# Performance work log

Hardware: AMD Instinct MI355X
Metric: run time of the kernel (lower is better)

## Reference

```python
import jax, jax.numpy as jnp
import numpy as np

B, SX, SL, D, H = 4, 4096, 256, 1024, 16
DH = D // H
LN_EPS = 1e-5
RMS_EPS = 1e-8


def layernorm(x, g, b):
    mu = jnp.mean(x, axis=-1, keepdims=True)
    var = jnp.mean(jnp.square(x - mu), axis=-1, keepdims=True)
    return (x - mu) * jax.lax.rsqrt(var + LN_EPS) * g + b


def rmsnorm(x, gamma):
    # torch: norm = ||x||_2 * dim^-0.5 ; x / clamp(norm, eps) * gamma
    norm = jnp.sqrt(jnp.sum(jnp.square(x), axis=-1, keepdims=True)) * (DH ** -0.5)
    return x / jnp.maximum(norm, RMS_EPS) * gamma


def setup_inputs() -> dict:
    key = jax.random.key(0)
    ks = jax.random.split(key, 6)
    s = 0.02
    return {
        "x": jax.random.normal(ks[0], (B, SX, D), jnp.float32),
        "latents": jax.random.normal(ks[1], (B, SL, D), jnp.float32),
        "mask_x": jnp.ones((B, SX), jnp.float32),
        "mask_latent": jnp.ones((B, SL), jnp.float32),
        "ln_x_g": jnp.ones((D,), jnp.float32),
        "ln_x_b": jnp.zeros((D,), jnp.float32),
        "ln_l_g": jnp.ones((D,), jnp.float32),
        "ln_l_b": jnp.zeros((D,), jnp.float32),
        "Wq": jax.random.normal(ks[2], (D, D), jnp.float32) * s,
        "Wkv": jax.random.normal(ks[3], (D, 2 * D), jnp.float32) * s,
        "qk_gamma": jnp.ones((DH,), jnp.float32),
        "Wo": jax.random.normal(ks[4], (D, D), jnp.float32) * s,
    }


def reference(x, latents, mask_x, mask_latent, ln_x_g, ln_x_b, ln_l_g, ln_l_b, Wq, Wkv, qk_gamma, Wo):
    xn = layernorm(x, ln_x_g, ln_x_b)                       # [B,SX,D]
    ln = layernorm(latents, ln_l_g, ln_l_b)                 # [B,SL,D]

    q = (ln @ Wq).reshape(B, SL, H, DH).transpose(0, 2, 1, 3)      # [B,H,SL,DH]
    kv_in = jnp.concatenate([xn, ln], axis=1)                      # [B,SX+SL,D]
    kv = kv_in @ Wkv
    Skv = SX + SL
    k = kv[..., :D].reshape(B, Skv, H, DH).transpose(0, 2, 1, 3)   # [B,H,Skv,DH]
    v = kv[..., D:].reshape(B, Skv, H, DH).transpose(0, 2, 1, 3)

    # NOTE: original code applies query_norm to BOTH q and k (faithful to source)
    q = rmsnorm(q, qk_gamma)
    k = rmsnorm(k, qk_gamma)

    scores = jnp.einsum("bhqd,bhkd->bhqk", q, k) / np.sqrt(DH)     # [B,H,SL,Skv]

    kv_mask = jnp.concatenate([mask_x, mask_latent], axis=1)       # [B,Skv]
    mask = kv_mask[:, None, :] * mask_latent[:, :, None]           # [B,SL,Skv]
    add_mask = (1.0 - mask)[:, None, :, :] * jnp.finfo(scores.dtype).min
    attn = jax.nn.softmax(scores + add_mask, axis=-1)

    y = jnp.einsum("bhqk,bhkd->bhqd", attn, v)                     # [B,H,SL,DH]
    y = y.transpose(0, 2, 1, 3).reshape(B, SL, D)
    return y @ Wo
```

## Files before the change

### kernel.cpp

```cpp
#include <hip/hip_runtime.h>

#define NB   4
#define SXX  4096
#define SLL  256
#define DD   1024
#define HH   16
#define DHH  64
#define SKV  4352
#define MKV  17408
#define NSPLIT 8

typedef __attribute__((ext_vector_type(8))) short bfrag;
typedef __attribute__((ext_vector_type(4))) float facc;

__device__ __forceinline__ unsigned short f2bf(float f){
  unsigned u = __builtin_bit_cast(unsigned, f);
  u = (u + 0x7fffu + ((u >> 16) & 1u)) >> 16;
  return (unsigned short)u;
}
__device__ __forceinline__ float bf2f(unsigned short h){
  unsigned u = ((unsigned)h) << 16;
  return __builtin_bit_cast(float, u);
}

#define GLOAD_LDS16(g, lds) __builtin_amdgcn_global_load_lds( \
    (const __attribute__((address_space(1))) unsigned int*)(const void*)(g), \
    (__attribute__((address_space(3))) unsigned int*)(void*)(lds), 16, 0, 0)

__global__ void wtrans3(const float* __restrict__ Wq, const float* __restrict__ Wkv,
                        const float* __restrict__ Wo, unsigned short* __restrict__ wqt,
                        unsigned short* __restrict__ wkvt, unsigned short* __restrict__ wot){
  __shared__ float t[32][33];
  int z = blockIdx.z;
  const float* in; unsigned short* out; int N;
  if (z == 0){ in = Wq;  out = wqt;  N = DD;   }
  else if (z == 1){ in = Wkv; out = wkvt; N = 2*DD; }
  else { in = Wo;  out = wot;  N = DD;   }
  int n0 = blockIdx.x * 32, k0 = blockIdx.y * 32;
  if (n0 >= N) return;
  int tx = threadIdx.x, ty = threadIdx.y;
  #pragma unroll
  for (int i = 0; i < 4; i++)
    t[ty + 8*i][tx] = in[(size_t)(k0 + ty + 8*i) * N + n0 + tx];
  __syncthreads();
  #pragma unroll
  for (int i = 0; i < 4; i++)
    out[(size_t)(n0 + ty + 8*i) * DD + k0 + tx] = f2bf(t[tx][ty + 8*i]);
}

__global__ __launch_bounds__(256) void lnorm2(const float* __restrict__ x,
    const float* __restrict__ lat,
    const float* __restrict__ gx, const float* __restrict__ bx,
    const float* __restrict__ gl, const float* __restrict__ bl,
    unsigned short* __restrict__ kvin, unsigned short* __restrict__ lnlat){
  int t = threadIdx.x, w = t >> 6, l = t & 63;
  int gr = blockIdx.x * 4 + w;
  const float* src; const float* g; const float* bt;
  unsigned short* d2 = nullptr;
  int b, s, off;
  if (gr < NB*SXX){
    b = gr >> 12; s = gr & 4095; off = 0;
    src = x + (size_t)gr * DD; g = gx; bt = bx;
  } else {
    int r = gr - NB*SXX;
    b = r >> 8; s = r & 255; off = SXX;
    src = lat + (size_t)r * DD; g = gl; bt = bl;
    d2 = lnlat + (size_t)r * DD;
  }
  const float4* rp = (const float4*)src;
  float4 v[4];
  float sum = 0.f, sq = 0.f;
  #pragma unroll
  for (int i = 0; i < 4; i++){
    v[i] = rp[l + i*64];
    sum += v[i].x + v[i].y + v[i].z + v[i].w;
    sq  += v[i].x*v[i].x + v[i].y*v[i].y + v[i].z*v[i].z + v[i].w*v[i].w;
  }
  #pragma unroll
  for (int o = 1; o < 64; o <<= 1){ sum += __shfl_xor(sum, o); sq += __shfl_xor(sq, o); }
  float mu = sum * (1.f/DD);
  float rs = rsqrtf(sq*(1.f/DD) - mu*mu + 1e-5f);
  unsigned short* dst = kvin + (size_t)(b*SKV + off + s) * DD;
  #pragma unroll
  for (int i = 0; i < 4; i++){
    float4 gv = ((const float4*)g)[l + i*64];
    float4 bv = ((const float4*)bt)[l + i*64];
    ushort4 o4;
    o4.x = f2bf((v[i].x - mu)*rs*gv.x + bv.x);
    o4.y = f2bf((v[i].y - mu)*rs*gv.y + bv.y);
    o4.z = f2bf((v[i].z - mu)*rs*gv.z + bv.z);
    o4.w = f2bf((v[i].w - mu)*rs*gv.w + bv.w);
    *(ushort4*)(dst + (size_t)(l + i*64)*4) = o4;
    if (d2) *(ushort4*)(d2 + (size_t)(l + i*64)*4) = o4;
  }
}

__global__ __launch_bounds__(256) void gemm64(const unsigned short* __restrict__ A,
    const unsigned short* __restrict__ Bt, int M, int N, int K, float* __restrict__ outF){
  __shared__ alignas(16) unsigned short lA[64*64];
  __shared__ alignas(16) unsigned short lB[64*64];
  int n0 = blockIdx.x * 64, m0 = blockIdx.y * 64;
  int t = threadIdx.x, w = t >> 6, l = t & 63;
  int wr = (w >> 1) * 32, wc = (w & 1) * 32;
  int lr = l & 15, q2 = l >> 4;
  int rA = w*8 + (l >> 3), u = l & 7;
  int swz = (u ^ (rA & 7)) * 8;
  const unsigned short* Ag = A  + (size_t)(m0 + rA) * K + swz;
  const unsigned short* Bg = Bt + (size_t)(n0 + rA) * K + swz;
  facc acc00 = (facc)0.f, acc01 = (facc)0.f, acc10 = (facc)0.f, acc11 = (facc)0.f;
  for (int k0 = 0; k0 < K; k0 += 64){
    GLOAD_LDS16(Ag + k0,                 &lA[(w*8)*64]);
    GLOAD_LDS16(Ag + (size_t)32*K + k0,  &lA[(32 + w*8)*64]);
    GLOAD_LDS16(Bg + k0,                 &lB[(w*8)*64]);
    GLOAD_LDS16(Bg + (size_t)32*K + k0,  &lB[(32 + w*8)*64]);
    __syncthreads();
    #pragma unroll
    for (int ks = 0; ks < 2; ks++){
      int cs = ((ks*4 + q2) ^ (lr & 7)) * 8;
      bfrag a0 = *(const bfrag*)&lA[(wr + lr)*64 + cs];
      bfrag a1 = *(const bfrag*)&lA[(wr + 16 + lr)*64 + cs];
      bfrag b0 = *(const bfrag*)&lB[(wc + lr)*64 + cs];
      bfrag b1 = *(const bfrag*)&lB[(wc + 16 + lr)*64 + cs];
      acc00 = __builtin_amdgcn_mfma_f32_16x16x32_bf16(a0, b0, acc00, 0, 0, 0);
      acc01 = __builtin_amdgcn_mfma_f32_16x16x32_bf16(a0, b1, acc01, 0, 0, 0);
      acc10 = __builtin_amdgcn_mfma_f32_16x16x32_bf16(a1, b0, acc10, 0, 0, 0);
      acc11 = __builtin_amdgcn_mfma_f32_16x16x32_bf16(a1, b1, acc11, 0, 0, 0);
    }
    __syncthreads();
  }
  int rl = (l >> 4) * 4, cl = l & 15;
  facc accs[2][2] = {{acc00, acc01},{acc10, acc11}};
  #pragma unroll
  for (int mt = 0; mt < 2; mt++)
  #pragma unroll
  for (int nt = 0; nt < 2; nt++)
  #pragma unroll
  for (int j = 0; j < 4; j++){
    int r = m0 + wr + mt*16 + rl + j;
    int c = n0 + wc + nt*16 + cl;
    outF[(size_t)r * N + c] = accs[mt][nt][j];
  }
}

__global__ __launch_bounds__(256) void gemm_q(const unsigned short* __restrict__ A,
    const unsigned short* __restrict__ Bt, const float* __restrict__ gamma,
    unsigned short* __restrict__ qn){
  __shared__ alignas(16) char smemb[18432];
  unsigned short* lA = (unsigned short*)smemb;
  unsigned short* lB = lA + 64*64;
  float* Cf = (float*)smemb;
  int h = blockIdx.x, n0 = h * 64, m0 = blockIdx.y * 64;
  int t = threadIdx.x, w = t >> 6, l = t & 63;
  int wr = (w >> 1) * 32, wc = (w & 1) * 32;
  int lr = l & 15, q2 = l >> 4;
  int rA = w*8 + (l >> 3), u = l & 7;
  int swz = (u ^ (rA & 7)) * 8;
  const unsigned short* Ag = A  + (size_t)(m0 + rA) * 1024 + swz;
  const unsigned short* Bg = Bt + (size_t)(n0 + rA) * 1024 + swz;
  facc acc00 = (facc)0.f, acc01 = (facc)0.f, acc10 = (facc)0.f, acc11 = (facc)0.f;
  for (int k0 = 0; k0 < 1024; k0 += 64){
    GLOAD_LDS16(Ag + k0,          &lA[(w*8)*64]);
    GLOAD_LDS16(Ag + 32768 + k0,  &lA[(32 + w*8)*64]);
    GLOAD_LDS16(Bg + k0,          &lB[(w*8)*64]);
    GLOAD_LDS16(Bg + 32768 + k0,  &lB[(32 + w*8)*64]);
    __syncthreads();
    #pragma unroll
    for (int ks = 0; ks < 2; ks++){
      int cs = ((ks*4 + q2) ^ (lr & 7)) * 8;
      bfrag a0 = *(const bfrag*)&lA[(wr + lr)*64 + cs];
      bfrag a1 = *(const bfrag*)&lA[(wr + 16 + lr)*64 + cs];
      bfrag b0 = *(const bfrag*)&lB[(wc + lr)*64 + cs];
      bfrag b1 = *(const bfrag*)&lB[(wc + 16 + lr)*64 + cs];
      acc00 = __builtin_amdgcn_mfma_f32_16x16x32_bf16(a0, b0, acc00, 0, 0, 0);
      acc01 = __builtin_amdgcn_mfma_f32_16x16x32_bf16(a0, b1, acc01, 0, 0, 0);
      acc10 = __builtin_amdgcn_mfma_f32_16x16x32_bf16(a1, b0, acc10, 0, 0, 0);
      acc11 = __builtin_amdgcn_mfma_f32_16x16x32_bf16(a1, b1, acc11, 0, 0, 0);
    }
    __syncthreads();
  }
  int rl = (l >> 4) * 4, cl = l & 15;
  facc accs[2][2] = {{acc00, acc01},{acc10, acc11}};
  #pragma unroll
  for (int mt = 0; mt < 2; mt++)
  #pragma unroll
  for (int nt = 0; nt < 2; nt++)
  #pragma unroll
  for (int j = 0; j < 4; j++)
    Cf[(wr + mt*16 + rl + j)*66 + wc + nt*16 + cl] = accs[mt][nt][j];
  __syncthreads();
  if (t < 64){
    const float* src = &Cf[t*66];
    float ss = 0.f;
    #pragma unroll
    for (int d = 0; d < 64; d++){ float a = src[d]; ss = fmaf(a, a, ss); }
    float rv = 0.125f / fmaxf(sqrtf(ss) * 0.125f, 1e-8f);
    int r = m0 + t, b = r >> 8, sl = r & 255;
    unsigned short* dst = &qn[((size_t)(b*HH + h)*SLL + sl)*DHH];
    #pragma unroll
    for (int i = 0; i < 8; i++){
      ushort4 p; float g;
      g = gamma[i*8+0]; p.x = f2bf(src[i*8+0]*g*g*rv);
      g = gamma[i*8+1]; p.y = f2bf(src[i*8+1]*g*g*rv);
      g = gamma[i*8+2]; p.z = f2bf(src[i*8+2]*g*g*rv);
      g = gamma[i*8+3]; p.w = f2bf(src[i*8+3]*g*g*rv);
      ushort4 q;
      g = gamma[i*8+4]; q.x = f2bf(src[i*8+4]*g*g*rv);
      g = gamma[i*8+5]; q.y = f2bf(src[i*8+5]*g*g*rv);
      g = gamma[i*8+6]; q.z = f2bf(src[i*8+6]*g*g*rv);
      g = gamma[i*8+7]; q.w = f2bf(src[i*8+7]*g*g*rv);
      *(ushort4*)&dst[i*8]     = p;
      *(ushort4*)&dst[i*8 + 4] = q;
    }
  }
}

__global__ __launch_bounds__(512, 2) void gemm_kv(const unsigned short* __restrict__ A,
    const unsigned short* __restrict__ Bt,
    const float* __restrict__ mask_x, const float* __restrict__ mask_lat,
    unsigned short* __restrict__ outK, unsigned short* __restrict__ outV,
    float* __restrict__ rkm){
  __shared__ alignas(16) unsigned short lds[3 * 24576];
  int bid = blockIdx.x;
  int wg = (bid & 7) * 136 + (bid >> 3);
  int m0 = (wg >> 4) * 256, n0 = (wg & 15) * 128;
  int t = threadIdx.x, w = t >> 6, l = t & 63;
  int wm = w >> 1, wn = w & 1;
  int lr = l & 15, q2 = l >> 4;
  int r8 = l >> 3, u = l & 7;
  int swz = (u ^ (r8 & 7)) * 8;
  const unsigned short* Ag = A  + (size_t)(m0 + w*8 + r8) * 1024 + swz;
  const unsigned short* Bg = Bt + (size_t)(n0 + w*8 + r8) * 1024 + swz;

  facc acc[4][4];
  #pragma unroll
  for (int mt = 0; mt < 4; mt++)
  #pragma unroll
  for (int nt = 0; nt < 4; nt++) acc[mt][nt] = (facc)0.f;

#define SBAR __builtin_amdgcn_sched_barrier(0)
#define KV_BARRIER do { SBAR; __builtin_amdgcn_s_barrier(); SBAR; } while(0)
#define KV_STA(j, i) GLOAD_LDS16(Ag + (size_t)(i)*65536 + (j)*64, \
    &lds[((j) % 3)*24576 + (i)*4096 + w*512])
#define KV_STB(j, i) GLOAD_LDS16(Bg + (size_t)(i)*65536 + (j)*64, \
    &lds[((j) % 3)*24576 + 16384 + (i)*4096 + w*512])
#define KV_LDF(va, vb, j, ks) { \
    const unsigned short* pA = &lds[((j) % 3)*24576 + (wm*64 + lr)*64 + (((ks)*4 + q2) ^ (lr & 7))*8]; \
    const unsigned short* pB = &lds[((j) % 3)*24576 + 16384 + (wn*64 + lr)*64 + (((ks)*4 + q2) ^ (lr & 7))*8]; \
    va[0] = *(const bfrag*)(pA);        va[1] = *(const bfrag*)(pA + 1024); \
    va[2] = *(const bfrag*)(pA + 2048); va[3] = *(const bfrag*)(pA + 3072); \
    vb[0] = *(const bfrag*)(pB);        vb[1] = *(const bfrag*)(pB + 1024); \
    vb[2] = *(const bfrag*)(pB + 2048); vb[3] = *(const bfrag*)(pB + 3072); }
#define KV_MFMA(va, vb) do { \
    __builtin_amdgcn_s_setprio(1); \
    _Pragma("unroll") \
    for (int mt = 0; mt < 4; mt++){ \
      _Pragma("unroll") \
      for (int nt = 0; nt < 4; nt++) \
        acc[mt][nt] = __builtin_amdgcn_mfma_f32_16x16x32_bf16(va[mt], vb[nt], acc[mt][nt], 0, 0, 0); } \
    __builtin_amdgcn_s_setprio(0); } while(0)

  KV_STA(0,0); KV_STA(0,1); KV_STA(0,2); KV_STA(0,3); KV_STB(0,0); KV_STB(0,1);
  KV_STA(1,0); KV_STA(1,1); KV_STA(1,2); KV_STA(1,3); KV_STB(1,0); KV_STB(1,1);
  __asm__ volatile("s_waitcnt vmcnt(6)" ::: "memory");
  KV_BARRIER;

  bfrag av[4], bv[4];
  #pragma unroll
  for (int j = 0; j < 16; j++){
    KV_LDF(av, bv, j, 0);
    if (j < 14){ KV_STA(j+2, 0); KV_STA(j+2, 1); KV_STB(j+2, 0); }
    KV_MFMA(av, bv);
    KV_LDF(av, bv, j, 1);
    if (j < 14){ KV_STA(j+2, 2); KV_STA(j+2, 3); KV_STB(j+2, 1); }
    KV_MFMA(av, bv);
    if (j < 14)       { __asm__ volatile("s_waitcnt vmcnt(6)" ::: "memory"); }
    else if (j == 14) { __asm__ volatile("s_waitcnt vmcnt(0)" ::: "memory"); }
    KV_BARRIER;
  }
#undef KV_STA
#undef KV_STB
#undef KV_LDF
#undef KV_MFMA

  int b = m0 / SKV, s0 = m0 - b*SKV;
  if (n0 < DD){
    #pragma unroll
    for (int mt = 0; mt < 4; mt++)
    #pragma unroll
    for (int nt = 0; nt < 4; nt++)
    #pragma unroll
    for (int j = 0; j < 4; j++)
      lds[(wm*64 + mt*16 + q2*4 + j)*136 + wn*64 + nt*16 + lr] = f2bf(acc[mt][nt][j]);
    __syncthreads();
    int s = t >> 1, hf = t & 1;
    int srow = s0 + s;
    float cm = (srow < SXX) ? mask_x[b*SXX + srow] : mask_lat[b*SLL + srow - SXX];
    const unsigned short* src = &lds[s*136 + hf*64];
    uint4 wv[8];
    #pragma unroll
    for (int i = 0; i < 8; i++) wv[i] = *(const uint4*)&src[i*8];
    float ss0 = 0.f, ss1 = 0.f;
    #pragma unroll
    for (int i = 0; i < 8; i++){
      const unsigned short* pp = (const unsigned short*)&wv[i];
      #pragma unroll
      for (int e = 0; e < 4; e++){
        float a = bf2f(pp[e]);     ss0 = fmaf(a, a, ss0);
        float c = bf2f(pp[e + 4]); ss1 = fmaf(c, c, ss1);
      }
    }
    float rv = 1.f / fmaxf(sqrtf(ss0 + ss1) * 0.125f, 1e-8f);
    int h = (n0 >> 6) + hf;
    unsigned short* dst = &outK[((size_t)(b*HH + h)*SKV + srow)*DHH];
    #pragma unroll
    for (int i = 0; i < 8; i++)
      *(uint4*)&dst[i*8] = wv[i];
    rkm[((size_t)(b*HH + h))*SKV + srow] = (cm != 0.f) ? rv : -1.f;
  } else {
    #pragma unroll
    for (int mt = 0; mt < 4; mt++)
    #pragma unroll
    for (int nt = 0; nt < 4; nt++){
      ushort4 p;
      p.x = f2bf(acc[mt][nt][0]); p.y = f2bf(acc[mt][nt][1]);
      p.z = f2bf(acc[mt][nt][2]); p.w = f2bf(acc[mt][nt][3]);
      *(ushort4*)&lds[(wn*64 + nt*16 + lr)*264 + wm*64 + mt*16 + q2*4] = p;
    }
    __syncthreads();
    int c = t >> 2, sq = t & 3;
    int hh = ((n0 - DD) >> 6) + (c >> 6), d = c & 63;
    const unsigned short* src = &lds[c*264 + sq*64];
    unsigned short* dst = &outV[((size_t)(b*HH + hh)*DHH + d)*SKV + s0 + sq*64];
    #pragma unroll
    for (int i = 0; i < 8; i++)
      *(uint4*)&dst[i*8] = *(const uint4*)&src[i*8];
  }
}

__global__ __launch_bounds__(256) void attn(const unsigned short* __restrict__ qn,
    const unsigned short* __restrict__ kbuf, const unsigned short* __restrict__ vT,
    const float* __restrict__ rkm, const float* __restrict__ mask_lat,
    float* __restrict__ Opart, float* __restrict__ lpart){
  int bh = blockIdx.y, split = blockIdx.z;
  int b = bh >> 4;
  __shared__ alignas(16) unsigned short lK[2][4096];
  __shared__ alignas(16) unsigned short lV[2][4096];
  __shared__ unsigned short lP[4][4][16][68];
  int t = threadIdx.x, w = t >> 6, l = t & 63;
  int lr = l & 15, q2 = l >> 4, kq = q2 * 8;
  int r8 = l >> 3, u = l & 7;
  int swz8 = (u ^ (r8 & 7)) * 8;
  int cs0 = (q2 ^ (lr & 7)) * 8;
  int cs1 = ((4 + q2) ^ (lr & 7)) * 8;
  const unsigned short* Kg = kbuf + ((size_t)bh*SKV + w*8 + r8)*DHH + swz8;
  const unsigned short* Vg = vT + (size_t)bh*DHH*SKV + (size_t)(w*8 + r8)*SKV + swz8;

  bfrag aq0[4], aq1[4];
  float rm[4][4];
  #pragma unroll
  for (int tt = 0; tt < 4; tt++){
    const unsigned short* qbase = qn + ((size_t)bh * SLL + tt*64 + w*16 + lr) * DHH;
    aq0[tt] = *(const bfrag*)&qbase[kq];
    aq1[tt] = *(const bfrag*)&qbase[32 + kq];
    #pragma unroll
    for (int j = 0; j < 4; j++) rm[tt][j] = mask_lat[b*SLL + tt*64 + w*16 + q2*4 + j];
  }
  facc O[4][4];
  #pragma unroll
  for (int tt = 0; tt < 4; tt++)
  #pragma unroll
  for (int nt = 0; nt < 4; nt++) O[tt][nt] = (facc)0.f;
  float lsum[4][4];
  #pragma unroll
  for (int tt = 0; tt < 4; tt++)
  #pragma unroll
  for (int j = 0; j < 4; j++) lsum[tt][j] = 0.f;

  int t0 = (split * 68) / NSPLIT, t1 = ((split + 1) * 68) / NSPLIT;
  {
    int key0 = t0 * 64;
    GLOAD_LDS16(Kg + (size_t)key0*DHH,          &lK[0][(w*8)*64]);
    GLOAD_LDS16(Kg + (size_t)(key0+32)*DHH,     &lK[0][(w*8 + 32)*64]);
    GLOAD_LDS16(Vg + key0,                      &lV[0][(w*8)*64]);
    GLOAD_LDS16(Vg + (size_t)32*SKV + key0,     &lV[0][(w*8 + 32)*64]);
  }
  __asm__ volatile("s_waitcnt vmcnt(0)" ::: "memory");
  __builtin_amdgcn_s_barrier();

  int p = 0;
  for (int kt = t0; kt < t1; kt++){
    int key0 = kt * 64;
    bfrag bk0[4], bk1[4], bv0[4], bv1[4]; float rk[4];
    #pragma unroll
    for (int nt = 0; nt < 4; nt++){
      const unsigned short* kr = &lK[p][(nt*16 + lr)*64];
      const unsigned short* vr = &lV[p][(nt*16 + lr)*64];
      bk0[nt] = *(const bfrag*)&kr[cs0];
      bk1[nt] = *(const bfrag*)&kr[cs1];
      bv0[nt] = *(const bfrag*)&vr[cs0];
      bv1[nt] = *(const bfrag*)&vr[cs1];
      rk[nt]  = rkm[(size_t)bh*SKV + key0 + nt*16 + lr];
    }
    if (kt + 1 < t1){
      int kn = key0 + 64;
      GLOAD_LDS16(Kg + (size_t)kn*DHH,        &lK[p^1][(w*8)*64]);
      GLOAD_LDS16(Kg + (size_t)(kn+32)*DHH,   &lK[p^1][(w*8 + 32)*64]);
      GLOAD_LDS16(Vg + kn,                    &lV[p^1][(w*8)*64]);
      GLOAD_LDS16(Vg + (size_t)32*SKV + kn,   &lV[p^1][(w*8 + 32)*64]);
    }
    #pragma unroll
    for (int tt = 0; tt < 4; tt++){
      facc S[4];
      #pragma unroll
      for (int nt = 0; nt < 4; nt++){
        S[nt] = (facc)0.f;
        S[nt] = __builtin_amdgcn_mfma_f32_16x16x32_bf16(aq0[tt], bk0[nt], S[nt], 0, 0, 0);
        S[nt] = __builtin_amdgcn_mfma_f32_16x16x32_bf16(aq1[tt], bk1[nt], S[nt], 0, 0, 0);
      }
      #pragma unroll
      for (int j = 0; j < 4; j++){
        float rs_ = 0.f;
        #pragma unroll
        for (int nt = 0; nt < 4; nt++){
          float x = S[nt][j] * rk[nt];
          float sv = (rk[nt] >= 0.f && rm[tt][j] != 0.f) ? x : -3.0e38f;
          float pz = __expf(sv - 8.0f);
          rs_ += pz;
          lP[w][tt][q2*4 + j][nt*16 + lr] = f2bf(pz);
        }
        lsum[tt][j] += rs_;
      }
    }
    __asm__ volatile("s_waitcnt lgkmcnt(0)" ::: "memory");
    #pragma unroll
    for (int tt = 0; tt < 4; tt++){
      bfrag ap0 = *(const bfrag*)&lP[w][tt][lr][kq];
      bfrag ap1 = *(const bfrag*)&lP[w][tt][lr][32 + kq];
      #pragma unroll
      for (int nt = 0; nt < 4; nt++){
        O[tt][nt] = __builtin_amdgcn_mfma_f32_16x16x32_bf16(ap0, bv0[nt], O[tt][nt], 0, 0, 0);
        O[tt][nt] = __builtin_amdgcn_mfma_f32_16x16x32_bf16(ap1, bv1[nt], O[tt][nt], 0, 0, 0);
      }
    }
    __asm__ volatile("s_waitcnt vmcnt(0)" ::: "memory");
    __builtin_amdgcn_s_barrier();
    p ^= 1;
  }
  #pragma unroll
  for (int tt = 0; tt < 4; tt++)
  #pragma unroll
  for (int j = 0; j < 4; j++){
    float L = lsum[tt][j];
    L += __shfl_xor(L, 1); L += __shfl_xor(L, 2);
    L += __shfl_xor(L, 4); L += __shfl_xor(L, 8);
    int srow = tt*64 + w*16 + q2*4 + j;
    size_t obase = (((size_t)split*64 + bh)*SLL + srow)*DHH;
    #pragma unroll
    for (int nt = 0; nt < 4; nt++)
      Opart[obase + nt*16 + lr] = O[tt][nt][j];
    if (lr == 0)
      lpart[((size_t)split*64 + bh)*SLL + srow] = L;
  }
}

__global__ __launch_bounds__(256) void attn_combine(const float* __restrict__ Opart,
    const float* __restrict__ lpart, unsigned short* __restrict__ ybuf){
  int t = threadIdx.x, w = t >> 6, l = t & 63;
  int idx = blockIdx.x * 4 + w;
  int bh = idx >> 8, srow = idx & 255;
  int b = bh >> 4, h = bh & 15;
  float L = 0.f, acc = 0.f;
  #pragma unroll
  for (int s = 0; s < NSPLIT; s++){
    L   += lpart[((size_t)s*64 + bh)*SLL + srow];
    acc += Opart[(((size_t)s*64 + bh)*SLL + srow)*DHH + l];
  }
  ybuf[((size_t)b*SLL + srow)*DD + h*DHH + l] = f2bf(acc / L);
}

extern "C" void kernel_launch(void* const* d_in, const int* in_sizes, int n_in,
                              void* d_out, int out_size, void* d_ws, size_t ws_size,
                              hipStream_t stream) {
  const float* x        = (const float*)d_in[0];
  const float* latents  = (const float*)d_in[1];
  const float* mask_x   = (const float*)d_in[2];
  const float* mask_lat = (const float*)d_in[3];
  const float* ln_x_g   = (const float*)d_in[4];
  const float* ln_x_b   = (const float*)d_in[5];
  const float* ln_l_g   = (const float*)d_in[6];
  const float* ln_l_b   = (const float*)d_in[7];
  const float* Wq       = (const float*)d_in[8];
  const float* Wkv      = (const float*)d_in[9];
  const float* qk_gamma = (const float*)d_in[10];
  const float* Wo       = (const float*)d_in[11];
  float* out = (float*)d_out;

  char* wsb = (char*)d_ws;
  unsigned short* kvin  = (unsigned short*)(wsb + 0);
  unsigned short* lnlat = (unsigned short*)(wsb + 35651584);
  unsigned short* wqt   = (unsigned short*)(wsb + 37748736);
  unsigned short* wkvt  = (unsigned short*)(wsb + 39845888);
  unsigned short* wot   = (unsigned short*)(wsb + 44040192);
  unsigned short* qnb   = (unsigned short*)(wsb + 50331648);
  unsigned short* kbuf  = (unsigned short*)(wsb + 52428800);
  unsigned short* vT    = (unsigned short*)(wsb + 88080384);
  float*          rkm   = (float*)(wsb + 123731968);
  unsigned short* ybuf  = (unsigned short*)(wsb + 124846080);
  float*          Opart = (float*)(wsb + 0);
  float*          lpart = (float*)(wsb + 35651584);

  wtrans3<<<dim3(64, 32, 3), dim3(32, 8), 0, stream>>>(Wq, Wkv, Wo, wqt, wkvt, wot);

  lnorm2<<<(NB*SXX + NB*SLL)/4, 256, 0, stream>>>(x, latents, ln_x_g, ln_x_b,
                                                  ln_l_g, ln_l_b, kvin, lnlat);

  gemm_q<<<dim3(16, 16), 256, 0, stream>>>(lnlat, wqt, qk_gamma, qnb);
  gemm_kv<<<dim3(1088), 512, 0, stream>>>(kvin, wkvt, mask_x, mask_lat, kbuf, vT, rkm);

  attn<<<dim3(1, NB*HH, NSPLIT), 256, 0, stream>>>(qnb, kbuf, vT, rkm, mask_lat, Opart, lpart);
  attn_combine<<<(NB*HH*SLL)/4, 256, 0, stream>>>(Opart, lpart, ybuf);

  gemm64<<<dim3(DD/64, (NB*SLL)/64), 256, 0, stream>>>(ybuf, wot, NB*SLL, DD, DD, out);
}
```

Measured before the change: 318.3 us.

## Merge weight transpose with layernorm and fold Q projection into KV GEMM

Merges the weight transpose/convert kernel and the layernorm kernel into one prep launch, partitioning blocks by index. Removes the separate Q GEMM kernel and instead appends 32 extra blocks to the KV GEMM grid. These blocks compute Q from the latent rows already in kvin using the transposed Wq, then apply the RMS norm in their epilogue. This cuts launches, removes the duplicate lnlat write, and lets Q work overlap the KV GEMM. In exchange, Q tiles use the larger 256x128 KV tiling, and the prep kernel mixes two different workloads in one launch.

```diff
diff --git a/kernel.cpp b/kernel.cpp
--- a/kernel.cpp
+++ b/kernel.cpp
@@ -27,71 +27,68 @@
     (const __attribute__((address_space(1))) unsigned int*)(const void*)(g), \
     (__attribute__((address_space(3))) unsigned int*)(void*)(lds), 16, 0, 0)
 
-__global__ void wtrans3(const float* __restrict__ Wq, const float* __restrict__ Wkv,
-                        const float* __restrict__ Wo, unsigned short* __restrict__ wqt,
-                        unsigned short* __restrict__ wkvt, unsigned short* __restrict__ wot){
-  __shared__ float t[32][33];
-  int z = blockIdx.z;
-  const float* in; unsigned short* out; int N;
-  if (z == 0){ in = Wq;  out = wqt;  N = DD;   }
-  else if (z == 1){ in = Wkv; out = wkvt; N = 2*DD; }
-  else { in = Wo;  out = wot;  N = DD;   }
-  int n0 = blockIdx.x * 32, k0 = blockIdx.y * 32;
-  if (n0 >= N) return;
-  int tx = threadIdx.x, ty = threadIdx.y;
-  #pragma unroll
-  for (int i = 0; i < 4; i++)
-    t[ty + 8*i][tx] = in[(size_t)(k0 + ty + 8*i) * N + n0 + tx];
-  __syncthreads();
-  #pragma unroll
-  for (int i = 0; i < 4; i++)
-    out[(size_t)(n0 + ty + 8*i) * DD + k0 + tx] = f2bf(t[tx][ty + 8*i]);
-}
-
-__global__ __launch_bounds__(256) void lnorm2(const float* __restrict__ x,
-    const float* __restrict__ lat,
+__global__ __launch_bounds__(256) void prep(const float* __restrict__ Wq,
+    const float* __restrict__ Wkv, const float* __restrict__ Wo,
+    unsigned short* __restrict__ wqt, unsigned short* __restrict__ wkvt,
+    unsigned short* __restrict__ wot,
+    const float* __restrict__ x, const float* __restrict__ lat,
     const float* __restrict__ gx, const float* __restrict__ bx,
     const float* __restrict__ gl, const float* __restrict__ bl,
-    unsigned short* __restrict__ kvin, unsigned short* __restrict__ lnlat){
-  int t = threadIdx.x, w = t >> 6, l = t & 63;
-  int gr = blockIdx.x * 4 + w;
-  const float* src; const float* g; const float* bt;
-  unsigned short* d2 = nullptr;
-  int b, s, off;
-  if (gr < NB*SXX){
-    b = gr >> 12; s = gr & 4095; off = 0;
-    src = x + (size_t)gr * DD; g = gx; bt = bx;
+    unsigned short* __restrict__ kvin){
+  __shared__ float tsh[32][33];
+  int bId = blockIdx.x;
+  int t = threadIdx.x;
+  if (bId < 4096){
+    const float* in; unsigned short* out; int N, n0, k0;
+    if (bId < 1024){ in = Wq;  out = wqt;  N = DD;   n0 = (bId & 31)*32; k0 = (bId >> 5)*32; }
+    else if (bId < 3072){ int b2 = bId - 1024; in = Wkv; out = wkvt; N = 2*DD; n0 = (b2 & 63)*32; k0 = (b2 >> 6)*32; }
+    else { int b3 = bId - 3072; in = Wo;  out = wot;  N = DD;   n0 = (b3 & 31)*32; k0 = (b3 >> 5)*32; }
+    int tx = t & 31, ty = t >> 5;
+    #pragma unroll
+    for (int i = 0; i < 4; i++)
+      tsh[ty + 8*i][tx] = in[(size_t)(k0 + ty + 8*i) * N + n0 + tx];
+    __syncthreads();
+    #pragma unroll
+    for (int i = 0; i < 4; i++)
+      out[(size_t)(n0 + ty + 8*i) * DD + k0 + tx] = f2bf(tsh[tx][ty + 8*i]);
   } else {
-    int r = gr - NB*SXX;
-    b = r >> 8; s = r & 255; off = SXX;
-    src = lat + (size_t)r * DD; g = gl; bt = bl;
-    d2 = lnlat + (size_t)r * DD;
-  }
-  const float4* rp = (const float4*)src;
-  float4 v[4];
-  float sum = 0.f, sq = 0.f;
-  #pragma unroll
-  for (int i = 0; i < 4; i++){
-    v[i] = rp[l + i*64];
-    sum += v[i].x + v[i].y + v[i].z + v[i].w;
-    sq  += v[i].x*v[i].x + v[i].y*v[i].y + v[i].z*v[i].z + v[i].w*v[i].w;
-  }
-  #pragma unroll
-  for (int o = 1; o < 64; o <<= 1){ sum += __shfl_xor(sum, o); sq += __shfl_xor(sq, o); }
-  float mu = sum * (1.f/DD);
-  float rs = rsqrtf(sq*(1.f/DD) - mu*mu + 1e-5f);
-  unsigned short* dst = kvin + (size_t)(b*SKV + off + s) * DD;
-  #pragma unroll
-  for (int i = 0; i < 4; i++){
-    float4 gv = ((const float4*)g)[l + i*64];
-    float4 bv = ((const float4*)bt)[l + i*64];
-    ushort4 o4;
-    o4.x = f2bf((v[i].x - mu)*rs*gv.x + bv.x);
-    o4.y = f2bf((v[i].y - mu)*rs*gv.y + bv.y);
-    o4.z = f2bf((v[i].z - mu)*rs*gv.z + bv.z);
-    o4.w = f2bf((v[i].w - mu)*rs*gv.w + bv.w);
-    *(ushort4*)(dst + (size_t)(l + i*64)*4) = o4;
-    if (d2) *(ushort4*)(d2 + (size_t)(l + i*64)*4) = o4;
+    int w = t >> 6, l = t & 63;
+    int gr = (bId - 4096) * 4 + w;
+    const float* src; const float* g; const float* bt;
+    int b, s, off;
+    if (gr < NB*SXX){
+      b = gr >> 12; s = gr & 4095; off = 0;
+      src = x + (size_t)gr * DD; g = gx; bt = bx;
+    } else {
+      int r = gr - NB*SXX;
+      b = r >> 8; s = r & 255; off = SXX;
+      src = lat + (size_t)r * DD; g = gl; bt = bl;
+    }
+    const float4* rp = (const float4*)src;
+    float4 v[4];
+    float sum = 0.f, sq = 0.f;
+    #pragma unroll
+    for (int i = 0; i < 4; i++){
+      v[i] = rp[l + i*64];
+      sum += v[i].x + v[i].y + v[i].z + v[i].w;
+      sq  += v[i].x*v[i].x + v[i].y*v[i].y + v[i].z*v[i].z + v[i].w*v[i].w;
+    }
+    #pragma unroll
+    for (int o = 1; o < 64; o <<= 1){ sum += __shfl_xor(sum, o); sq += __shfl_xor(sq, o); }
+    float mu = sum * (1.f/DD);
+    float rs = rsqrtf(sq*(1.f/DD) - mu*mu + 1e-5f);
+    unsigned short* dst = kvin + (size_t)(b*SKV + off + s) * DD;
+    #pragma unroll
+    for (int i = 0; i < 4; i++){
+      float4 gv = ((const float4*)g)[l + i*64];
+      float4 bv = ((const float4*)bt)[l + i*64];
+      ushort4 o4;
+      o4.x = f2bf((v[i].x - mu)*rs*gv.x + bv.x);
+      o4.y = f2bf((v[i].y - mu)*rs*gv.y + bv.y);
+      o4.z = f2bf((v[i].z - mu)*rs*gv.z + bv.z);
+      o4.w = f2bf((v[i].w - mu)*rs*gv.w + bv.w);
+      *(ushort4*)(dst + (size_t)(l + i*64)*4) = o4;
+    }
   }
 }
 
@@ -142,94 +139,34 @@
   }
 }
 
-__global__ __launch_bounds__(256) void gemm_q(const unsigned short* __restrict__ A,
-    const unsigned short* __restrict__ Bt, const float* __restrict__ gamma,
-    unsigned short* __restrict__ qn){
-  __shared__ alignas(16) char smemb[18432];
-  unsigned short* lA = (unsigned short*)smemb;
-  unsigned short* lB = lA + 64*64;
-  float* Cf = (float*)smemb;
-  int h = blockIdx.x, n0 = h * 64, m0 = blockIdx.y * 64;
-  int t = threadIdx.x, w = t >> 6, l = t & 63;
-  int wr = (w >> 1) * 32, wc = (w & 1) * 32;
-  int lr = l & 15, q2 = l >> 4;
-  int rA = w*8 + (l >> 3), u = l & 7;
-  int swz = (u ^ (rA & 7)) * 8;
-  const unsigned short* Ag = A  + (size_t)(m0 + rA) * 1024 + swz;
-  const unsigned short* Bg = Bt + (size_t)(n0 + rA) * 1024 + swz;
-  facc acc00 = (facc)0.f, acc01 = (facc)0.f, acc10 = (facc)0.f, acc11 = (facc)0.f;
-  for (int k0 = 0; k0 < 1024; k0 += 64){
-    GLOAD_LDS16(Ag + k0,          &lA[(w*8)*64]);
-    GLOAD_LDS16(Ag + 32768 + k0,  &lA[(32 + w*8)*64]);
-    GLOAD_LDS16(Bg + k0,          &lB[(w*8)*64]);
-    GLOAD_LDS16(Bg + 32768 + k0,  &lB[(32 + w*8)*64]);
-    __syncthreads();
-    #pragma unroll
-    for (int ks = 0; ks < 2; ks++){
-      int cs = ((ks*4 + q2) ^ (lr & 7)) * 8;
-      bfrag a0 = *(const bfrag*)&lA[(wr + lr)*64 + cs];
-      bfrag a1 = *(const bfrag*)&lA[(wr + 16 + lr)*64 + cs];
-      bfrag b0 = *(const bfrag*)&lB[(wc + lr)*64 + cs];
-      bfrag b1 = *(const bfrag*)&lB[(wc + 16 + lr)*64 + cs];
-      acc00 = __builtin_amdgcn_mfma_f32_16x16x32_bf16(a0, b0, acc00, 0, 0, 0);
-      acc01 = __builtin_amdgcn_mfma_f32_16x16x32_bf16(a0, b1, acc01, 0, 0, 0);
-      acc10 = __builtin_amdgcn_mfma_f32_16x16x32_bf16(a1, b0, acc10, 0, 0, 0);
-      acc11 = __builtin_amdgcn_mfma_f32_16x16x32_bf16(a1, b1, acc11, 0, 0, 0);
-    }
-    __syncthreads();
-  }
-  int rl = (l >> 4) * 4, cl = l & 15;
-  facc accs[2][2] = {{acc00, acc01},{acc10, acc11}};
-  #pragma unroll
-  for (int mt = 0; mt < 2; mt++)
-  #pragma unroll
-  for (int nt = 0; nt < 2; nt++)
-  #pragma unroll
-  for (int j = 0; j < 4; j++)
-    Cf[(wr + mt*16 + rl + j)*66 + wc + nt*16 + cl] = accs[mt][nt][j];
-  __syncthreads();
-  if (t < 64){
-    const float* src = &Cf[t*66];
-    float ss = 0.f;
-    #pragma unroll
-    for (int d = 0; d < 64; d++){ float a = src[d]; ss = fmaf(a, a, ss); }
-    float rv = 0.125f / fmaxf(sqrtf(ss) * 0.125f, 1e-8f);
-    int r = m0 + t, b = r >> 8, sl = r & 255;
-    unsigned short* dst = &qn[((size_t)(b*HH + h)*SLL + sl)*DHH];
-    #pragma unroll
-    for (int i = 0; i < 8; i++){
-      ushort4 p; float g;
-      g = gamma[i*8+0]; p.x = f2bf(src[i*8+0]*g*g*rv);
-      g = gamma[i*8+1]; p.y = f2bf(src[i*8+1]*g*g*rv);
-      g = gamma[i*8+2]; p.z = f2bf(src[i*8+2]*g*g*rv);
-      g = gamma[i*8+3]; p.w = f2bf(src[i*8+3]*g*g*rv);
-      ushort4 q;
-      g = gamma[i*8+4]; q.x = f2bf(src[i*8+4]*g*g*rv);
-      g = gamma[i*8+5]; q.y = f2bf(src[i*8+5]*g*g*rv);
-      g = gamma[i*8+6]; q.z = f2bf(src[i*8+6]*g*g*rv);
-      g = gamma[i*8+7]; q.w = f2bf(src[i*8+7]*g*g*rv);
-      *(ushort4*)&dst[i*8]     = p;
-      *(ushort4*)&dst[i*8 + 4] = q;
-    }
-  }
-}
-
 __global__ __launch_bounds__(512, 2) void gemm_kv(const unsigned short* __restrict__ A,
-    const unsigned short* __restrict__ Bt,
+    const unsigned short* __restrict__ Bt, const unsigned short* __restrict__ Wqt,
+    const float* __restrict__ gamma,
     const float* __restrict__ mask_x, const float* __restrict__ mask_lat,
     unsigned short* __restrict__ outK, unsigned short* __restrict__ outV,
-    float* __restrict__ rkm){
+    float* __restrict__ rkm, unsigned short* __restrict__ qn){
   __shared__ alignas(16) unsigned short lds[3 * 24576];
   int bid = blockIdx.x;
-  int wg = (bid & 7) * 136 + (bid >> 3);
-  int m0 = (wg >> 4) * 256, n0 = (wg & 15) * 128;
+  int m0, n0;
+  const unsigned short* Bbase;
+  bool isQ = bid >= 1088;
+  if (!isQ){
+    int wg = (bid & 7) * 136 + (bid >> 3);
+    m0 = (wg >> 4) * 256; n0 = (wg & 15) * 128;
+    Bbase = Bt;
+  } else {
+    int i = bid - 1088;
+    m0 = (i >> 3) * SKV + SXX;
+    n0 = (i & 7) * 128;
+    Bbase = Wqt;
+  }
   int t = threadIdx.x, w = t >> 6, l = t & 63;
   int wm = w >> 1, wn = w & 1;
   int lr = l & 15, q2 = l >> 4;
   int r8 = l >> 3, u = l & 7;
   int swz = (u ^ (r8 & 7)) * 8;
-  const unsigned short* Ag = A  + (size_t)(m0 + w*8 + r8) * 1024 + swz;
-  const unsigned short* Bg = Bt + (size_t)(n0 + w*8 + r8) * 1024 + swz;
+  const unsigned short* Ag = A     + (size_t)(m0 + w*8 + r8) * 1024 + swz;
+  const unsigned short* Bg = Bbase + (size_t)(n0 + w*8 + r8) * 1024 + swz;
 
   facc acc[4][4];
   #pragma unroll
@@ -282,6 +219,43 @@
 #undef KV_LDF
 #undef KV_MFMA
 
+  if (isQ){
+    int qb = (bid - 1088) >> 3;
+    float* ldsF = (float*)lds;
+    #pragma unroll
+    for (int mt = 0; mt < 4; mt++)
+    #pragma unroll
+    for (int nt = 0; nt < 4; nt++)
+    #pragma unroll
+    for (int j = 0; j < 4; j++)
+      ldsF[(wm*64 + mt*16 + q2*4 + j)*132 + wn*64 + nt*16 + lr] = acc[mt][nt][j];
+    __syncthreads();
+    int s = t >> 1, hf = t & 1;
+    const float* src = &ldsF[s*132 + hf*64];
+    float ss = 0.f;
+    #pragma unroll
+    for (int d = 0; d < 64; d++){ float a = src[d]; ss = fmaf(a, a, ss); }
+    float rv = 0.125f / fmaxf(sqrtf(ss) * 0.125f, 1e-8f);
+    int h = (n0 >> 6) + hf;
+    unsigned short* dst = &qn[((size_t)(qb*HH + h)*SLL + s)*DHH];
+    #pragma unroll
+    for (int i = 0; i < 8; i++){
+      ushort4 p; float g;
+      g = gamma[i*8+0]; p.x = f2bf(src[i*8+0]*g*g*rv);
+      g = gamma[i*8+1]; p.y = f2bf(src[i*8+1]*g*g*rv);
+      g = gamma[i*8+2]; p.z = f2bf(src[i*8+2]*g*g*rv);
+      g = gamma[i*8+3]; p.w = f2bf(src[i*8+3]*g*g*rv);
+      ushort4 q;
+      g = gamma[i*8+4]; q.x = f2bf(src[i*8+4]*g*g*rv);
+      g = gamma[i*8+5]; q.y = f2bf(src[i*8+5]*g*g*rv);
+      g = gamma[i*8+6]; q.z = f2bf(src[i*8+6]*g*g*rv);
+      g = gamma[i*8+7]; q.w = f2bf(src[i*8+7]*g*g*rv);
+      *(ushort4*)&dst[i*8]     = p;
+      *(ushort4*)&dst[i*8 + 4] = q;
+    }
+    return;
+  }
+
   int b = m0 / SKV, s0 = m0 - b*SKV;
   if (n0 < DD){
     #pragma unroll
@@ -497,7 +471,6 @@
 
   char* wsb = (char*)d_ws;
   unsigned short* kvin  = (unsigned short*)(wsb + 0);
-  unsigned short* lnlat = (unsigned short*)(wsb + 35651584);
   unsigned short* wqt   = (unsigned short*)(wsb + 37748736);
   unsigned short* wkvt  = (unsigned short*)(wsb + 39845888);
   unsigned short* wot   = (unsigned short*)(wsb + 44040192);
@@ -509,13 +482,11 @@
   float*          Opart = (float*)(wsb + 0);
   float*          lpart = (float*)(wsb + 35651584);
 
-  wtrans3<<<dim3(64, 32, 3), dim3(32, 8), 0, stream>>>(Wq, Wkv, Wo, wqt, wkvt, wot);
-
-  lnorm2<<<(NB*SXX + NB*SLL)/4, 256, 0, stream>>>(x, latents, ln_x_g, ln_x_b,
-                                                  ln_l_g, ln_l_b, kvin, lnlat);
-
-  gemm_q<<<dim3(16, 16), 256, 0, stream>>>(lnlat, wqt, qk_gamma, qnb);
-  gemm_kv<<<dim3(1088), 512, 0, stream>>>(kvin, wkvt, mask_x, mask_lat, kbuf, vT, rkm);
+  prep<<<8448, 256, 0, stream>>>(Wq, Wkv, Wo, wqt, wkvt, wot,
+                                 x, latents, ln_x_g, ln_x_b, ln_l_g, ln_l_b, kvin);
+
+  gemm_kv<<<dim3(1120), 512, 0, stream>>>(kvin, wkvt, wqt, qk_gamma,
+                                          mask_x, mask_lat, kbuf, vT, rkm, qnb);
 
   attn<<<dim3(1, NB*HH, NSPLIT), 256, 0, stream>>>(qnb, kbuf, vT, rkm, mask_lat, Opart, lpart);
   attn_combine<<<(NB*HH*SLL)/4, 256, 0, stream>>>(Opart, lpart, ybuf);
```

New measurement: 307.0 us, median of 2. 1.04x faster.
